# Kernel optimization log

Hardware: AMD Instinct MI355X
Metric: run time of the kernel (lower is better)

The kernel has to match this reference:

```python
import jax, jax.numpy as jnp
import numpy as np

D_MODEL = 256
N_HEAD = 8
HEAD_DIM = D_MODEL // N_HEAD
N_TOTAL = 24576
B, T = 64, 512


def setup_inputs() -> dict:
    key = jax.random.key(0)
    ks = jax.random.split(key, 12)
    s = 1.0 / np.sqrt(D_MODEL)
    return {
        "x": jax.random.normal(ks[0], (N_TOTAL, D_MODEL), jnp.float32),
        "Wq": jax.random.uniform(ks[1], (D_MODEL, D_MODEL), jnp.float32, -s, s),
        "bq": jax.random.uniform(ks[2], (D_MODEL,), jnp.float32, -s, s),
        "Wk": jax.random.uniform(ks[3], (D_MODEL, D_MODEL), jnp.float32, -s, s),
        "bk": jax.random.uniform(ks[4], (D_MODEL,), jnp.float32, -s, s),
        "Wv": jax.random.uniform(ks[5], (D_MODEL, D_MODEL), jnp.float32, -s, s),
        "bv": jax.random.uniform(ks[6], (D_MODEL,), jnp.float32, -s, s),
        "Wp": jax.random.uniform(ks[7], (D_MODEL, D_MODEL), jnp.float32, -s, s),
        "bp": jax.random.uniform(ks[8], (D_MODEL,), jnp.float32, -s, s),
        "padpack_index": jax.random.randint(ks[9], (B, T), 0, N_TOTAL, jnp.int64 if jax.config.jax_enable_x64 else jnp.int32),
        "padpack_batch": jax.random.randint(ks[10], (B, T), 0, B, jnp.int32),
        "padpack_inverse_index": jax.random.randint(ks[11], (N_TOTAL,), 0, B * T, jnp.int64 if jax.config.jax_enable_x64 else jnp.int32),
    }


def reference(x, Wq, bq, Wk, bk, Wv, bv, Wp, bp, padpack_index, padpack_batch, padpack_inverse_index):
    # gather ragged tokens into packed [B, T, C]
    xp = x[padpack_index]
    # mask: True where packed slots share the same segment id (matches
    # original masked_fill(batch_i == batch_j, -1e9))
    mask = padpack_batch[:, :, None] == padpack_batch[:, None, :]  # [B,T,T]
    # QKV projections (torch Linear: x @ W.T + b), split heads
    def heads(w, b):
        h = xp @ w.T + b
        return h.reshape(B, T, N_HEAD, HEAD_DIM).transpose(0, 2, 1, 3)  # [B,H,T,D]
    q, k, v = heads(Wq, bq), heads(Wk, bk), heads(Wv, bv)
    att = jnp.einsum("bhtd,bhsd->bhts", q, k) * (1.0 / np.sqrt(HEAD_DIM))
    att = jnp.where(mask[:, None], jnp.float32(-1e9), att)
    att = jax.nn.softmax(att, axis=-1)
    y = jnp.einsum("bhts,bhsd->bhtd", att, v)  # [B,H,T,D]
    y = y.transpose(0, 2, 1, 3).reshape(B, T, D_MODEL)
    y = y @ Wp.T + bp
    # scatter back to ragged layout
    return y.reshape(B * T, D_MODEL)[padpack_inverse_index]
```

## Files before the change

### kernel.cpp

```cpp
#include <hip/hip_runtime.h>


typedef __attribute__((ext_vector_type(8))) short short8;
typedef __attribute__((ext_vector_type(4))) float f32x4;

#define N_TOTAL 24576
#define B_ 64
#define T_ 512
#define DM 256
#define NH 8
#define HD 32
#define F3 768

#define QSCALE 0.25503463f
#define VSP 530

__device__ __forceinline__ unsigned short f2bf(float f) {
  unsigned int u = __float_as_uint(f);
  u += 0x7fffu + ((u >> 16) & 1u);
  return (unsigned short)(u >> 16);
}

__device__ __forceinline__ void gl_lds16(const void* g, void* l) {
  __builtin_amdgcn_global_load_lds(
      (const __attribute__((address_space(1))) unsigned int*)g,
      (__attribute__((address_space(3))) unsigned int*)l, 16, 0, 0);
}

__global__ __launch_bounds__(256) void pack_kernel(
    const float* __restrict__ x, const float* __restrict__ Wq,
    const float* __restrict__ Wk, const float* __restrict__ Wv,
    const float* __restrict__ Wp, const float* __restrict__ bq,
    const float* __restrict__ bk, const float* __restrict__ bv,
    const int* __restrict__ idx,
    short* __restrict__ XP, short* __restrict__ WCAT, short* __restrict__ WPb,
    float* __restrict__ BCAT) {
  int gid = blockIdx.x * 256 + threadIdx.x;
  if (gid < 768)
    BCAT[gid] = (gid < 256) ? bq[gid] : (gid < 512 ? bk[gid - 256] : bv[gid - 512]);
  const float* src;
  short* dst;
  if (gid < 1048576) {
    int row = gid >> 5, seg = gid & 31;
    src = x + (size_t)idx[row] * DM + seg * 8;
    dst = XP + (size_t)gid * 8;
  } else if (gid < 1073152) {
    int u = gid - 1048576;
    int f = u >> 5, seg = u & 31;
    const float* W = (f < 256) ? Wq : ((f < 512) ? Wk : Wv);
    src = W + (size_t)(f & 255) * DM + seg * 8;
    dst = WCAT + (size_t)u * 8;
  } else {
    int u = gid - 1073152;
    src = Wp + (size_t)u * 8;
    dst = WPb + (size_t)u * 8;
  }
  const float4* s4 = (const float4*)src;
  float4 a = s4[0], b = s4[1];
  short8 o;
  o[0] = (short)f2bf(a.x); o[1] = (short)f2bf(a.y);
  o[2] = (short)f2bf(a.z); o[3] = (short)f2bf(a.w);
  o[4] = (short)f2bf(b.x); o[5] = (short)f2bf(b.y);
  o[6] = (short)f2bf(b.z); o[7] = (short)f2bf(b.w);
  *(short8*)dst = o;
}

__global__ __launch_bounds__(256) void qkv_gemm(
    const short* __restrict__ XP, const short* __restrict__ WCAT,
    const float* __restrict__ BCAT, unsigned short* __restrict__ QKVp) {
  __shared__ __align__(16) char smem[3 * 16384];
  int tid = threadIdx.x;
  int lane = tid & 63, w = tid >> 6;
  int i = lane & 15, q = lane >> 4;
  int m0 = blockIdx.x * 128, n0 = blockIdx.y * 128;
  int wm = (w & 1) * 64, wn = (w >> 1) * 64;
  int csa = q ^ ((i >> 1) & 3);

  f32x4 zf = {0.f, 0.f, 0.f, 0.f};
  f32x4 acc[4][4];
#pragma unroll
  for (int mt = 0; mt < 4; mt++)
#pragma unroll
    for (int nt = 0; nt < 4; nt++) acc[mt][nt] = zf;

  auto stage = [&](int k, int s) {
#pragma unroll
    for (int p = 0; p < 2; p++) {
      int U = p * 256 + tid;
      int row = U >> 2, c = U & 3;
      int cs = c ^ ((row >> 1) & 3);
      gl_lds16(XP + (size_t)(m0 + row) * DM + k * 32 + cs * 8,
               smem + s * 16384 + U * 16);
      gl_lds16(WCAT + (size_t)(n0 + row) * DM + k * 32 + cs * 8,
               smem + s * 16384 + 8192 + U * 16);
    }
  };

  stage(0, 0);
  stage(1, 1);
#pragma unroll
  for (int k = 0; k < 8; k++) {
    if (k == 7)
      asm volatile("s_waitcnt vmcnt(0) lgkmcnt(0)\ns_barrier" ::: "memory");
    else
      asm volatile("s_waitcnt vmcnt(4) lgkmcnt(0)\ns_barrier" ::: "memory");
    const short* Asb = (const short*)(smem + (k % 3) * 16384);
    const short* Bsb = Asb + 4096;
    short8 a[4], bfr[4];
#pragma unroll
    for (int mt = 0; mt < 4; mt++)
      a[mt] = *(const short8*)&Asb[(wm + mt * 16 + i) * 32 + csa * 8];
#pragma unroll
    for (int nt = 0; nt < 4; nt++)
      bfr[nt] = *(const short8*)&Bsb[(wn + nt * 16 + i) * 32 + csa * 8];
    if (k < 6) stage(k + 2, (k + 2) % 3);
#pragma unroll
    for (int mt = 0; mt < 4; mt++)
#pragma unroll
      for (int nt = 0; nt < 4; nt++)
        acc[mt][nt] = __builtin_amdgcn_mfma_f32_16x16x32_bf16(a[mt], bfr[nt], acc[mt][nt], 0, 0, 0);
  }

  float scale = (n0 < 256) ? QSCALE : 1.0f;
#pragma unroll
  for (int nt = 0; nt < 4; nt++) {
    int f = n0 + wn + nt * 16 + i;
    float bias = BCAT[f];
#pragma unroll
    for (int mt = 0; mt < 4; mt++) {
#pragma unroll
      for (int r = 0; r < 4; r++) {
        int token = m0 + wm + mt * 16 + q * 4 + r;
        QKVp[(size_t)token * F3 + f] = f2bf((acc[mt][nt][r] + bias) * scale);
      }
    }
  }
}

__global__ __launch_bounds__(512, 4) void attn_kernel(
    const unsigned short* __restrict__ QKVp, const int* __restrict__ batch,
    unsigned short* __restrict__ Y) {
  __shared__ __align__(16) short Vl[HD * VSP];
  __shared__ int sbat[T_];
  int tid = threadIdx.x, w = tid >> 6, lane = tid & 63;
  int i = lane & 15, q = lane >> 4;
  int bx = blockIdx.x;
  int h = bx >> 6, b = bx & 63;
  int t0 = w * 64;
  const unsigned short* Tok = QKVp + (size_t)b * T_ * F3;

  sbat[tid] = batch[b * T_ + tid];

  {
    int seg = tid & 3, sb = tid >> 2;
#pragma unroll
    for (int l = 0; l < 4; l++) {
      int s = sb + l * 128;
      short8 v = *(const short8*)&Tok[(size_t)s * F3 + 512 + h * HD + seg * 8];
#pragma unroll
      for (int j = 0; j < 8; j++) Vl[(seg * 8 + j) * VSP + s] = v[j];
    }
  }
  __syncthreads();

  short8 qf[4];
  int btm[4];
#pragma unroll
  for (int mt = 0; mt < 4; mt++)
    qf[mt] = *(const short8*)&Tok[(size_t)(t0 + mt * 16 + i) * F3 + h * HD + q * 8];
#pragma unroll
  for (int mt = 0; mt < 4; mt++) btm[mt] = sbat[t0 + mt * 16 + i];

  unsigned short ob = (i == 0) ? (unsigned short)0x3F80 : (unsigned short)0;
  short8 ones = {(short)ob, (short)ob, (short)ob, (short)ob,
                 (short)ob, (short)ob, (short)ob, (short)ob};

  f32x4 zf = {0.f, 0.f, 0.f, 0.f};
  f32x4 o[4][2], lacc[4];
#pragma unroll
  for (int mt = 0; mt < 4; mt++) {
    o[mt][0] = zf; o[mt][1] = zf; lacc[mt] = zf;
  }

  const unsigned short* Kb = Tok + 256 + h * HD + q * 8;
  short8 k0f = *(const short8*)&Kb[(size_t)(i)*F3];
  short8 k1f = *(const short8*)&Kb[(size_t)(16 + i) * F3];

  for (int s0 = 0; s0 < T_; s0 += 32) {
    short8 ck0 = k0f, ck1 = k1f;
    if (s0 + 32 < T_) {
      k0f = *(const short8*)&Kb[(size_t)(s0 + 32 + i) * F3];
      k1f = *(const short8*)&Kb[(size_t)(s0 + 48 + i) * F3];
    }
    int4 bs0 = *(const int4*)&sbat[s0 + q * 4];
    int4 bs1 = *(const int4*)&sbat[s0 + 16 + q * 4];
    short8 v0f = *(const short8*)&Vl[i * VSP + s0 + q * 8];
    short8 v1f = *(const short8*)&Vl[(16 + i) * VSP + s0 + q * 8];
#pragma unroll
    for (int mt = 0; mt < 4; mt++) {
      f32x4 st0 = __builtin_amdgcn_mfma_f32_16x16x32_bf16(ck0, qf[mt], zf, 0, 0, 0);
      f32x4 st1 = __builtin_amdgcn_mfma_f32_16x16x32_bf16(ck1, qf[mt], zf, 0, 0, 0);
      int bm = btm[mt];
      float e00 = __builtin_amdgcn_exp2f((bs0.x == bm) ? -1e9f : st0[0]);
      float e01 = __builtin_amdgcn_exp2f((bs0.y == bm) ? -1e9f : st0[1]);
      float e02 = __builtin_amdgcn_exp2f((bs0.z == bm) ? -1e9f : st0[2]);
      float e03 = __builtin_amdgcn_exp2f((bs0.w == bm) ? -1e9f : st0[3]);
      float e10 = __builtin_amdgcn_exp2f((bs1.x == bm) ? -1e9f : st1[0]);
      float e11 = __builtin_amdgcn_exp2f((bs1.y == bm) ? -1e9f : st1[1]);
      float e12 = __builtin_amdgcn_exp2f((bs1.z == bm) ? -1e9f : st1[2]);
      float e13 = __builtin_amdgcn_exp2f((bs1.w == bm) ? -1e9f : st1[3]);
      unsigned A0 = __builtin_amdgcn_perm(__float_as_uint(e01), __float_as_uint(e00), 0x07060302u);
      unsigned A1 = __builtin_amdgcn_perm(__float_as_uint(e03), __float_as_uint(e02), 0x07060302u);
      unsigned B0 = __builtin_amdgcn_perm(__float_as_uint(e11), __float_as_uint(e10), 0x07060302u);
      unsigned B1 = __builtin_amdgcn_perm(__float_as_uint(e13), __float_as_uint(e12), 0x07060302u);
      asm volatile(
          "s_nop 1\n\t"
          "v_permlane32_swap_b32 %0, %2\n\t"
          "v_permlane32_swap_b32 %1, %3\n\t"
          "s_nop 1\n\t"
          "v_permlane16_swap_b32 %0, %2\n\t"
          "v_permlane16_swap_b32 %1, %3\n\t"
          "s_nop 1"
          : "+v"(A0), "+v"(A1), "+v"(B0), "+v"(B1));
      union {
        unsigned u[4];
        short8 s;
      } cv;
      cv.u[0] = A0;
      cv.u[1] = A1;
      cv.u[2] = B0;
      cv.u[3] = B1;
      short8 pa = cv.s;
      o[mt][0] = __builtin_amdgcn_mfma_f32_16x16x32_bf16(pa, v0f, o[mt][0], 0, 0, 0);
      o[mt][1] = __builtin_amdgcn_mfma_f32_16x16x32_bf16(pa, v1f, o[mt][1], 0, 0, 0);
      lacc[mt] = __builtin_amdgcn_mfma_f32_16x16x32_bf16(pa, ones, lacc[mt], 0, 0, 0);
    }
  }

#pragma unroll
  for (int mt = 0; mt < 4; mt++) {
#pragma unroll
    for (int r = 0; r < 4; r++) {
      float lv = __shfl(lacc[mt][r], lane & 48, 64);
      float inv = __builtin_amdgcn_rcpf(lv);
      size_t yb = ((size_t)b * T_ + t0 + mt * 16 + q * 4 + r) * DM + h * HD;
      Y[yb + i] = f2bf(o[mt][0][r] * inv);
      Y[yb + 16 + i] = f2bf(o[mt][1][r] * inv);
    }
  }
}

__global__ __launch_bounds__(256) void out_gemm(
    const short* __restrict__ Y, const short* __restrict__ WPb,
    const float* __restrict__ bp, const int* __restrict__ inv,
    float* __restrict__ out) {
  __shared__ __align__(16) char smem[3 * 16384];
  int tid = threadIdx.x;
  int lane = tid & 63, w = tid >> 6;
  int i = lane & 15, q = lane >> 4;
  int m0 = blockIdx.x * 128, n0 = blockIdx.y * 128;
  int wm = (w & 1) * 64, wn = (w >> 1) * 64;
  int csa = q ^ ((i >> 1) & 3);

  int iv0 = inv[m0 + (tid >> 2)];
  int iv1 = inv[m0 + 64 + (tid >> 2)];

  f32x4 zf = {0.f, 0.f, 0.f, 0.f};
  f32x4 acc[4][4];
#pragma unroll
  for (int mt = 0; mt < 4; mt++)
#pragma unroll
    for (int nt = 0; nt < 4; nt++) acc[mt][nt] = zf;

  auto stage = [&](int k, int s) {
#pragma unroll
    for (int p = 0; p < 2; p++) {
      int U = p * 256 + tid;
      int row = U >> 2, c = U & 3;
      int cs = c ^ ((row >> 1) & 3);
      int iv = p ? iv1 : iv0;
      gl_lds16(Y + (size_t)iv * DM + k * 32 + cs * 8, smem + s * 16384 + U * 16);
      gl_lds16(WPb + (size_t)(n0 + row) * DM + k * 32 + cs * 8,
               smem + s * 16384 + 8192 + U * 16);
    }
  };

  stage(0, 0);
  stage(1, 1);
#pragma unroll
  for (int k = 0; k < 8; k++) {
    if (k == 7)
      asm volatile("s_waitcnt vmcnt(0) lgkmcnt(0)\ns_barrier" ::: "memory");
    else
      asm volatile("s_waitcnt vmcnt(4) lgkmcnt(0)\ns_barrier" ::: "memory");
    const short* Asb = (const short*)(smem + (k % 3) * 16384);
    const short* Bsb = Asb + 4096;
    short8 a[4], bfr[4];
#pragma unroll
    for (int mt = 0; mt < 4; mt++)
      a[mt] = *(const short8*)&Asb[(wm + mt * 16 + i) * 32 + csa * 8];
#pragma unroll
    for (int nt = 0; nt < 4; nt++)
      bfr[nt] = *(const short8*)&Bsb[(wn + nt * 16 + i) * 32 + csa * 8];
    if (k < 6) stage(k + 2, (k + 2) % 3);
#pragma unroll
    for (int mt = 0; mt < 4; mt++)
#pragma unroll
      for (int nt = 0; nt < 4; nt++)
        acc[mt][nt] = __builtin_amdgcn_mfma_f32_16x16x32_bf16(a[mt], bfr[nt], acc[mt][nt], 0, 0, 0);
  }

#pragma unroll
  for (int nt = 0; nt < 4; nt++) {
    int f = n0 + wn + nt * 16 + i;
    float bias = bp[f];
#pragma unroll
    for (int mt = 0; mt < 4; mt++) {
#pragma unroll
      for (int r = 0; r < 4; r++) {
        int row = m0 + wm + mt * 16 + q * 4 + r;
        out[(size_t)row * DM + f] = acc[mt][nt][r] + bias;
      }
    }
  }
}

extern "C" void kernel_launch(void* const* d_in, const int* in_sizes, int n_in,
                              void* d_out, int out_size, void* d_ws, size_t ws_size,
                              hipStream_t stream) {
  const float* x = (const float*)d_in[0];
  const float* Wq = (const float*)d_in[1];
  const float* bq = (const float*)d_in[2];
  const float* Wk = (const float*)d_in[3];
  const float* bk = (const float*)d_in[4];
  const float* Wv = (const float*)d_in[5];
  const float* bv = (const float*)d_in[6];
  const float* Wp = (const float*)d_in[7];
  const float* bp = (const float*)d_in[8];
  const int* idx = (const int*)d_in[9];
  const int* batch = (const int*)d_in[10];
  const int* inv = (const int*)d_in[11];
  float* out = (float*)d_out;

  char* ws = (char*)d_ws;
  short* XP = (short*)(ws + 0);
  short* WCAT = (short*)(ws + 16777216);
  short* WPb = (short*)(ws + 17170432);
  float* BCAT = (float*)(ws + 17301504);
  unsigned short* QKVp = (unsigned short*)(ws + 17304576);
  unsigned short* Yb = (unsigned short*)(ws + 67636224);

  pack_kernel<<<4224, 256, 0, stream>>>(x, Wq, Wk, Wv, Wp, bq, bk, bv, idx,
                                        XP, WCAT, WPb, BCAT);
  qkv_gemm<<<dim3(256, 6), 256, 0, stream>>>(XP, WCAT, BCAT, QKVp);
  attn_kernel<<<512, 512, 0, stream>>>(QKVp, batch, Yb);
  out_gemm<<<dim3(192, 2), 256, 0, stream>>>((const short*)Yb, WPb, bp, inv, out);
}
```

Before: 169.1 us.

## Fuse row gather and bf16 conversion of x into QKV GEMM loads

Removes the packed bf16 XP intermediate: the QKV GEMM now gathers fp32 rows of x by index into registers, converts them to bf16 and writes them into LDS, pipelined alongside the async weight loads. The pack kernel now only converts weights and biases. This saves a full write and read of the packed activation buffer, but each GEMM column block re-reads fp32 x, doubling its bytes and adding conversion ALU work in the main loop.

```diff
diff --git a/kernel.cpp b/kernel.cpp
--- a/kernel.cpp
+++ b/kernel.cpp
@@ -28,30 +28,24 @@
 }
 
 __global__ __launch_bounds__(256) void pack_kernel(
-    const float* __restrict__ x, const float* __restrict__ Wq,
-    const float* __restrict__ Wk, const float* __restrict__ Wv,
-    const float* __restrict__ Wp, const float* __restrict__ bq,
-    const float* __restrict__ bk, const float* __restrict__ bv,
-    const int* __restrict__ idx,
-    short* __restrict__ XP, short* __restrict__ WCAT, short* __restrict__ WPb,
+    const float* __restrict__ Wq, const float* __restrict__ Wk,
+    const float* __restrict__ Wv, const float* __restrict__ Wp,
+    const float* __restrict__ bq, const float* __restrict__ bk,
+    const float* __restrict__ bv,
+    short* __restrict__ WCAT, short* __restrict__ WPb,
     float* __restrict__ BCAT) {
   int gid = blockIdx.x * 256 + threadIdx.x;
   if (gid < 768)
     BCAT[gid] = (gid < 256) ? bq[gid] : (gid < 512 ? bk[gid - 256] : bv[gid - 512]);
   const float* src;
   short* dst;
-  if (gid < 1048576) {
-    int row = gid >> 5, seg = gid & 31;
-    src = x + (size_t)idx[row] * DM + seg * 8;
-    dst = XP + (size_t)gid * 8;
-  } else if (gid < 1073152) {
-    int u = gid - 1048576;
-    int f = u >> 5, seg = u & 31;
+  if (gid < 24576) {
+    int f = gid >> 5, seg = gid & 31;
     const float* W = (f < 256) ? Wq : ((f < 512) ? Wk : Wv);
     src = W + (size_t)(f & 255) * DM + seg * 8;
-    dst = WCAT + (size_t)u * 8;
+    dst = WCAT + (size_t)gid * 8;
   } else {
-    int u = gid - 1073152;
+    int u = gid - 24576;
     src = Wp + (size_t)u * 8;
     dst = WPb + (size_t)u * 8;
   }
@@ -66,8 +60,9 @@
 }
 
 __global__ __launch_bounds__(256) void qkv_gemm(
-    const short* __restrict__ XP, const short* __restrict__ WCAT,
-    const float* __restrict__ BCAT, unsigned short* __restrict__ QKVp) {
+    const float* __restrict__ x, const int* __restrict__ idx,
+    const short* __restrict__ WCAT, const float* __restrict__ BCAT,
+    unsigned short* __restrict__ QKVp) {
   __shared__ __align__(16) char smem[3 * 16384];
   int tid = threadIdx.x;
   int lane = tid & 63, w = tid >> 6;
@@ -76,6 +71,13 @@
   int wm = (w & 1) * 64, wn = (w >> 1) * 64;
   int csa = q ^ ((i >> 1) & 3);
 
+  int row0 = tid >> 2, c = tid & 3;
+  int row1 = 64 + row0;
+  int cs0 = c ^ ((row0 >> 1) & 3);
+  int cs1 = c ^ ((row1 >> 1) & 3);
+  const float* ax0 = x + (size_t)idx[m0 + row0] * DM;
+  const float* ax1 = x + (size_t)idx[m0 + row1] * DM;
+
   f32x4 zf = {0.f, 0.f, 0.f, 0.f};
   f32x4 acc[4][4];
 #pragma unroll
@@ -83,27 +85,49 @@
 #pragma unroll
     for (int nt = 0; nt < 4; nt++) acc[mt][nt] = zf;
 
-  auto stage = [&](int k, int s) {
-#pragma unroll
-    for (int p = 0; p < 2; p++) {
-      int U = p * 256 + tid;
-      int row = U >> 2, c = U & 3;
-      int cs = c ^ ((row >> 1) & 3);
-      gl_lds16(XP + (size_t)(m0 + row) * DM + k * 32 + cs * 8,
-               smem + s * 16384 + U * 16);
-      gl_lds16(WCAT + (size_t)(n0 + row) * DM + k * 32 + cs * 8,
-               smem + s * 16384 + 8192 + U * 16);
-    }
+  float4 fa[2][2][2];
+
+  auto issueA = [&](int k, int par) {
+    fa[par][0][0] = *(const float4*)(ax0 + k * 32 + cs0 * 8);
+    fa[par][0][1] = *(const float4*)(ax0 + k * 32 + cs0 * 8 + 4);
+    fa[par][1][0] = *(const float4*)(ax1 + k * 32 + cs1 * 8);
+    fa[par][1][1] = *(const float4*)(ax1 + k * 32 + cs1 * 8 + 4);
   };
-
-  stage(0, 0);
-  stage(1, 1);
+  auto issueB = [&](int k, int s) {
+    gl_lds16(WCAT + (size_t)(n0 + row0) * DM + k * 32 + cs0 * 8,
+             smem + s * 16384 + 8192 + tid * 16);
+    gl_lds16(WCAT + (size_t)(n0 + row1) * DM + k * 32 + cs1 * 8,
+             smem + s * 16384 + 8192 + (256 + tid) * 16);
+  };
+  auto writeA = [&](int s, int par) {
+    short8 o0, o1;
+    float4 l0 = fa[par][0][0], h0 = fa[par][0][1];
+    float4 l1 = fa[par][1][0], h1 = fa[par][1][1];
+    o0[0] = (short)f2bf(l0.x); o0[1] = (short)f2bf(l0.y);
+    o0[2] = (short)f2bf(l0.z); o0[3] = (short)f2bf(l0.w);
+    o0[4] = (short)f2bf(h0.x); o0[5] = (short)f2bf(h0.y);
+    o0[6] = (short)f2bf(h0.z); o0[7] = (short)f2bf(h0.w);
+    o1[0] = (short)f2bf(l1.x); o1[1] = (short)f2bf(l1.y);
+    o1[2] = (short)f2bf(l1.z); o1[3] = (short)f2bf(l1.w);
+    o1[4] = (short)f2bf(h1.x); o1[5] = (short)f2bf(h1.y);
+    o1[6] = (short)f2bf(h1.z); o1[7] = (short)f2bf(h1.w);
+    *(short8*)(smem + s * 16384 + tid * 16) = o0;
+    *(short8*)(smem + s * 16384 + (256 + tid) * 16) = o1;
+  };
+
+  issueA(0, 0);
+  issueB(0, 0);
+  issueA(1, 1);
+  issueB(1, 1);
+  asm volatile("s_waitcnt vmcnt(8)" ::: "memory");
+  writeA(0, 0);
+
 #pragma unroll
   for (int k = 0; k < 8; k++) {
     if (k == 7)
       asm volatile("s_waitcnt vmcnt(0) lgkmcnt(0)\ns_barrier" ::: "memory");
     else
-      asm volatile("s_waitcnt vmcnt(4) lgkmcnt(0)\ns_barrier" ::: "memory");
+      asm volatile("s_waitcnt vmcnt(6) lgkmcnt(0)\ns_barrier" ::: "memory");
     const short* Asb = (const short*)(smem + (k % 3) * 16384);
     const short* Bsb = Asb + 4096;
     short8 a[4], bfr[4];
@@ -113,12 +137,22 @@
 #pragma unroll
     for (int nt = 0; nt < 4; nt++)
       bfr[nt] = *(const short8*)&Bsb[(wn + nt * 16 + i) * 32 + csa * 8];
-    if (k < 6) stage(k + 2, (k + 2) % 3);
+    if (k < 6) {
+      issueA(k + 2, k & 1);
+      issueB(k + 2, (k + 2) % 3);
+    }
 #pragma unroll
     for (int mt = 0; mt < 4; mt++)
 #pragma unroll
       for (int nt = 0; nt < 4; nt++)
         acc[mt][nt] = __builtin_amdgcn_mfma_f32_16x16x32_bf16(a[mt], bfr[nt], acc[mt][nt], 0, 0, 0);
+    if (k < 7) {
+      if (k < 6)
+        asm volatile("s_waitcnt vmcnt(8)" ::: "memory");
+      else
+        asm volatile("s_waitcnt vmcnt(2)" ::: "memory");
+      writeA((k + 1) % 3, (k + 1) & 1);
+    }
   }
 
   float scale = (n0 < 256) ? QSCALE : 1.0f;
@@ -343,16 +377,15 @@
   float* out = (float*)d_out;
 
   char* ws = (char*)d_ws;
-  short* XP = (short*)(ws + 0);
-  short* WCAT = (short*)(ws + 16777216);
-  short* WPb = (short*)(ws + 17170432);
-  float* BCAT = (float*)(ws + 17301504);
-  unsigned short* QKVp = (unsigned short*)(ws + 17304576);
-  unsigned short* Yb = (unsigned short*)(ws + 67636224);
-
-  pack_kernel<<<4224, 256, 0, stream>>>(x, Wq, Wk, Wv, Wp, bq, bk, bv, idx,
-                                        XP, WCAT, WPb, BCAT);
-  qkv_gemm<<<dim3(256, 6), 256, 0, stream>>>(XP, WCAT, BCAT, QKVp);
+  short* WCAT = (short*)(ws + 0);
+  short* WPb = (short*)(ws + 524288);
+  float* BCAT = (float*)(ws + 1048576);
+  unsigned short* QKVp = (unsigned short*)(ws + 2097152);
+  unsigned short* Yb = (unsigned short*)(ws + 52428800);
+
+  pack_kernel<<<128, 256, 0, stream>>>(Wq, Wk, Wv, Wp, bq, bk, bv,
+                                       WCAT, WPb, BCAT);
+  qkv_gemm<<<dim3(256, 6), 256, 0, stream>>>(x, idx, WCAT, BCAT, QKVp);
   attn_kernel<<<512, 512, 0, stream>>>(QKVp, batch, Yb);
   out_gemm<<<dim3(192, 2), 256, 0, stream>>>((const short*)Yb, WPb, bp, inv, out);
 }
```

Result: faster. 163.9 us, median of 2 (-3.1%).
